# Kernel tuning notes

Measured on AMD Instinct MI355X. Metric: run time of the kernel, lower is better.

Reference implementation:

```python
import jax, jax.numpy as jnp
import numpy as np

NORMALIZE_EPS = 1e-5
INV_DELTA = 15.0
DIST_NORM_PREV = 0.5  # init value of _dist_norm_prev buffer (eval-mode constant)
SKIP_OFFSET = 2


def _l2_normalize(v, axis, eps=NORMALIZE_EPS):
    # matches torch F.normalize: v / max(||v||, eps)
    n = jnp.sqrt(jnp.sum(v * v, axis=axis, keepdims=True))
    return v / jnp.maximum(n, eps)


def setup_inputs() -> dict:
    key = jax.random.key(0)
    k1, k2 = jax.random.split(key)
    x = jax.random.normal(k1, (128, 197, 768), dtype=jnp.float32)
    emb = jnp.clip(jax.random.normal(k2, (4096, 768), dtype=jnp.float32), 0.0, None)
    emb = _l2_normalize(emb, axis=1)
    return {"x": x, "embedding": emb}


def reference(x, embedding):
    # drop CLS token -> [N, L, C] with L = H*W
    x = x[:, 1:, :]
    N, L, C = x.shape
    height = width = int(np.sqrt(L))
    # assign_words: L2-normalize tokens, cosine distance to codebook
    xn = _l2_normalize(x, axis=2)
    dist = -jnp.einsum("nlc,kc->nlk", xn, embedding)  # [N, L, K]
    inv_delta = INV_DELTA / DIST_NORM_PREV
    codes = jax.nn.softmax(-inv_delta * dist, axis=2)  # [N, L, K]
    # compute_bow: drop border tokens, mean-pool, L1-normalize
    grid = jnp.arange(height * width).reshape(height, width)
    keep = grid[SKIP_OFFSET:-SKIP_OFFSET, SKIP_OFFSET:-SKIP_OFFSET].reshape(-1)
    bow = jnp.mean(codes[:, keep, :], axis=1)  # [N, K]
    bow = bow / jnp.maximum(jnp.sum(jnp.abs(bow), axis=1, keepdims=True), NORMALIZE_EPS)
    return bow, codes
```

## Files before the change

kernel.cpp:

```cpp
#include <hip/hip_runtime.h>


typedef unsigned short ushort_t;
typedef short short8 __attribute__((ext_vector_type(8)));
typedef float float4_ __attribute__((ext_vector_type(4)));

#define M_ROWS 25088
#define N_COLS 4096
#define K_DIM  768
#define BM 128
#define BN 128
#define BK 32

__device__ __forceinline__ unsigned short f2bf_rne(float f) {
  unsigned u = __float_as_uint(f);
  unsigned r = u + 0x7fffu + ((u >> 16) & 1u);
  return (unsigned short)(r >> 16);
}
__device__ __forceinline__ float bf2f(unsigned short h) {
  return __uint_as_float(((unsigned)h) << 16);
}

__device__ __forceinline__ void gload16(const void* g, void* l) {
  __builtin_amdgcn_global_load_lds(
      (__attribute__((address_space(1))) void*)g,
      (__attribute__((address_space(3))) void*)l, 16, 0, 0);
}

__global__ void split_emb_kernel(const float* __restrict__ emb,
                                 ushort_t* __restrict__ Bh,
                                 ushort_t* __restrict__ Bl) {
  int t = blockIdx.x * 256 + threadIdx.x;
  float f = emb[t];
  unsigned short h = f2bf_rne(f);
  Bh[t] = h;
  Bl[t] = f2bf_rne(f - bf2f(h));
}

__global__ void norm_split_x_kernel(const float* __restrict__ x,
                                    ushort_t* __restrict__ Ah,
                                    ushort_t* __restrict__ Al) {
  int m = blockIdx.x;
  int n = m / 196;
  int l = m - n * 196;
  size_t src = ((size_t)n * 197 + 1 + l) * 768;
  int t = threadIdx.x;

  float v0 = x[src + t];
  float v1 = x[src + t + 256];
  float v2 = x[src + t + 512];
  float s = v0 * v0 + v1 * v1 + v2 * v2;
  #pragma unroll
  for (int off = 32; off; off >>= 1) s += __shfl_xor(s, off, 64);
  __shared__ float ws4[4];
  if ((t & 63) == 0) ws4[t >> 6] = s;
  __syncthreads();
  s = ws4[0] + ws4[1] + ws4[2] + ws4[3];
  float scale = 1.0f / fmaxf(sqrtf(s), 1e-5f);

  size_t dst = (size_t)m * 768;
  float f[3] = {v0 * scale, v1 * scale, v2 * scale};
  int idx[3] = {t, t + 256, t + 512};
  #pragma unroll
  for (int i = 0; i < 3; i++) {
    unsigned short h = f2bf_rne(f[i]);
    Ah[dst + idx[i]] = h;
    Al[dst + idx[i]] = f2bf_rne(f[i] - bf2f(h));
  }
}

__global__ __launch_bounds__(256, 4)
void gemm_exp_kernel(const ushort_t* __restrict__ Ah, const ushort_t* __restrict__ Al,
                     const ushort_t* __restrict__ Bh, const ushort_t* __restrict__ Bl,
                     float* __restrict__ codes, float* __restrict__ rowsum) {
  __shared__ __attribute__((aligned(16))) ushort_t sAh[BM * BK];
  __shared__ __attribute__((aligned(16))) ushort_t sAl[BM * BK];
  __shared__ __attribute__((aligned(16))) ushort_t sBh[BM * BK];
  __shared__ __attribute__((aligned(16))) ushort_t sBl[BM * BK];
  __shared__ float rs[BM];

  const int t = threadIdx.x;
  const int w = t >> 6;
  const int lane = t & 63;
  const int row0 = blockIdx.x * BM;
  const int col0 = blockIdx.y * BN;

  if (t < BM) rs[t] = 0.f;

  float4_ acc[4][4];
  #pragma unroll
  for (int i = 0; i < 4; i++)
    #pragma unroll
    for (int j = 0; j < 4; j++) acc[i][j] = (float4_){0.f, 0.f, 0.f, 0.f};

  const int r0 = t >> 2;
  const int c0 = (((t & 3) ^ ((r0 >> 1) & 3))) * 8;
  const ushort_t* gA = Ah + (size_t)(row0 + r0) * K_DIM + c0;
  const ushort_t* gAl_ = Al + (size_t)(row0 + r0) * K_DIM + c0;
  const ushort_t* gB = Bh + (size_t)(col0 + r0) * K_DIM + c0;
  const ushort_t* gBl_ = Bl + (size_t)(col0 + r0) * K_DIM + c0;
  const int half = 64 * K_DIM;
  const int ldsw = w * 512;

  const int rl = (w >> 1) * 64;
  const int cl = (w & 1) * 64;
  const int lq = lane >> 4;
  const int li = lane & 15;
  const int fsw = (li >> 1) & 3;
  const int abase = (rl + li) * BK + (lq ^ fsw) * 8;
  const int bbase = (cl + li) * BK + (lq ^ fsw) * 8;

  for (int kk = 0; kk < K_DIM; kk += BK) {
    __syncthreads();
    gload16(gA + kk,           sAh + ldsw);
    gload16(gA + kk + half,    sAh + 2048 + ldsw);
    gload16(gAl_ + kk,         sAl + ldsw);
    gload16(gAl_ + kk + half,  sAl + 2048 + ldsw);
    gload16(gB + kk,           sBh + ldsw);
    gload16(gB + kk + half,    sBh + 2048 + ldsw);
    gload16(gBl_ + kk,         sBl + ldsw);
    gload16(gBl_ + kk + half,  sBl + 2048 + ldsw);
    __syncthreads();

    short8 ah[4], al[4], bh[4], bl[4];
    #pragma unroll
    for (int i = 0; i < 4; i++) {
      ah[i] = *(const short8*)(sAh + abase + i * 16 * BK);
      al[i] = *(const short8*)(sAl + abase + i * 16 * BK);
      bh[i] = *(const short8*)(sBh + bbase + i * 16 * BK);
      bl[i] = *(const short8*)(sBl + bbase + i * 16 * BK);
    }
    #pragma unroll
    for (int i = 0; i < 4; i++)
      #pragma unroll
      for (int j = 0; j < 4; j++) {
        acc[i][j] = __builtin_amdgcn_mfma_f32_16x16x32_bf16(ah[i], bh[j], acc[i][j], 0, 0, 0);
        acc[i][j] = __builtin_amdgcn_mfma_f32_16x16x32_bf16(ah[i], bl[j], acc[i][j], 0, 0, 0);
        acc[i][j] = __builtin_amdgcn_mfma_f32_16x16x32_bf16(al[i], bh[j], acc[i][j], 0, 0, 0);
      }
  }

  float rsum[4][4];
  #pragma unroll
  for (int i = 0; i < 4; i++)
    #pragma unroll
    for (int r = 0; r < 4; r++) rsum[i][r] = 0.f;

  #pragma unroll
  for (int i = 0; i < 4; i++)
    #pragma unroll
    for (int j = 0; j < 4; j++)
      #pragma unroll
      for (int r = 0; r < 4; r++) {
        float e = __expf(30.0f * acc[i][j][r]);
        size_t row = (size_t)(row0 + rl + i * 16 + lq * 4 + r);
        size_t col = (size_t)(col0 + cl + j * 16 + li);
        codes[row * N_COLS + col] = e;
        rsum[i][r] += e;
      }

  #pragma unroll
  for (int i = 0; i < 4; i++)
    #pragma unroll
    for (int r = 0; r < 4; r++) {
      float v = rsum[i][r];
      v += __shfl_xor(v, 1, 64);
      v += __shfl_xor(v, 2, 64);
      v += __shfl_xor(v, 4, 64);
      v += __shfl_xor(v, 8, 64);
      if (li == 0) atomicAdd(&rs[rl + i * 16 + lq * 4 + r], v);
    }
  __syncthreads();
  if (t < BM) atomicAdd(&rowsum[row0 + t], rs[t]);
}

__global__ __launch_bounds__(256)
void rescale_bow_kernel(float* __restrict__ codes,
                        const float* __restrict__ rowsum,
                        float* __restrict__ bow_un) {
  const int bid = blockIdx.x;
  const int n = bid >> 4;
  const int g = (bid >> 2) & 3;
  const int chunk = bid & 3;
  const int t = threadIdx.x;
  const int k4 = chunk * 256 + t;
  const int l0 = g * 49;

  __shared__ float inv[49];
  __shared__ float keep[49];
  if (t < 49) {
    int l = l0 + t;
    inv[t] = 1.0f / rowsum[n * 196 + l];
    int rr = l / 14;
    int cc = l - rr * 14;
    keep[t] = (rr >= 2 && rr <= 11 && cc >= 2 && cc <= 11) ? 0.01f : 0.0f;
  }
  __syncthreads();

  float4_* base = (float4_*)(codes + (size_t)n * 196 * N_COLS)
                  + (size_t)l0 * 1024 + k4;
  float4_ acc = {0.f, 0.f, 0.f, 0.f};
  #pragma unroll
  for (int c = 0; c < 7; c++) {
    float4_ v[7];
    #pragma unroll
    for (int u = 0; u < 7; u++) v[u] = base[(size_t)(c * 7 + u) * 1024];
    #pragma unroll
    for (int u = 0; u < 7; u++) {
      int l = c * 7 + u;
      float iv = inv[l];
      v[u].x *= iv; v[u].y *= iv; v[u].z *= iv; v[u].w *= iv;
      base[(size_t)l * 1024] = v[u];
      float kf = keep[l];
      acc.x += kf * v[u].x; acc.y += kf * v[u].y;
      acc.z += kf * v[u].z; acc.w += kf * v[u].w;
    }
  }

  float* dst = bow_un + (size_t)n * N_COLS + (size_t)k4 * 4;
  atomicAdd(dst + 0, acc.x);
  atomicAdd(dst + 1, acc.y);
  atomicAdd(dst + 2, acc.z);
  atomicAdd(dst + 3, acc.w);
}

__global__ __launch_bounds__(256)
void bow_norm_kernel(const float* __restrict__ bow_un,
                     float* __restrict__ bow_out) {
  const int n = blockIdx.x;
  const int t = threadIdx.x;
  const float4_* src = (const float4_*)(bow_un + (size_t)n * N_COLS);
  float4_ v[4];
  float s = 0.f;
  #pragma unroll
  for (int i = 0; i < 4; i++) {
    v[i] = src[t + i * 256];
    s += fabsf(v[i].x) + fabsf(v[i].y) + fabsf(v[i].z) + fabsf(v[i].w);
  }
  #pragma unroll
  for (int off = 32; off; off >>= 1) s += __shfl_xor(s, off, 64);
  __shared__ float ws4[4];
  if ((t & 63) == 0) ws4[t >> 6] = s;
  __syncthreads();
  float invn = 1.0f / fmaxf(ws4[0] + ws4[1] + ws4[2] + ws4[3], 1e-5f);
  float4_* dst = (float4_*)(bow_out + (size_t)n * N_COLS);
  #pragma unroll
  for (int i = 0; i < 4; i++) {
    float4_ o = v[i];
    o.x *= invn; o.y *= invn; o.z *= invn; o.w *= invn;
    dst[t + i * 256] = o;
  }
}

extern "C" void kernel_launch(void* const* d_in, const int* in_sizes, int n_in,
                              void* d_out, int out_size, void* d_ws, size_t ws_size,
                              hipStream_t stream) {
  const float* x = (const float*)d_in[0];
  const float* emb = (const float*)d_in[1];
  float* bow_out = (float*)d_out;
  float* codes = (float*)d_out + 524288;

  char* ws = (char*)d_ws;
  ushort_t* Ah = (ushort_t*)(ws + 0);
  ushort_t* Al = (ushort_t*)(ws + 38535168);
  ushort_t* Bh = (ushort_t*)(ws + 77070336);
  ushort_t* Bl = (ushort_t*)(ws + 83361792);
  float* rowsum = (float*)(ws + 89653248);
  float* bow_un = (float*)(ws + 89753600);

  hipMemsetAsync(rowsum, 0, 25088 * 4, stream);
  hipMemsetAsync(bow_un, 0, 524288 * 4, stream);

  split_emb_kernel<<<12288, 256, 0, stream>>>(emb, Bh, Bl);
  norm_split_x_kernel<<<25088, 256, 0, stream>>>(x, Ah, Al);

  dim3 ggrid(M_ROWS / BM, N_COLS / BN);
  gemm_exp_kernel<<<ggrid, 256, 0, stream>>>(Ah, Al, Bh, Bl, codes, rowsum);

  rescale_bow_kernel<<<2048, 256, 0, stream>>>(codes, rowsum, bow_un);
  bow_norm_kernel<<<128, 256, 0, stream>>>(bow_un, bow_out);
}
```

Baseline: 1.121 ms.

## Double-buffer LDS tiles to overlap global loads with MFMA compute

The GEMM's shared-memory tiles are split into two buffers. The next K-slice is loaded with async global-to-LDS loads while the current slice is multiplied, using vmcnt waits and raw barriers in place of the two __syncthreads per step. This is meant to hide global load latency behind the split-bf16 MFMA work. LDS use doubles to 64KB and the launch bound drops to 2 blocks per CU, so occupancy falls.

```diff
diff --git a/kernel.cpp b/kernel.cpp
--- a/kernel.cpp
+++ b/kernel.cpp
@@ -11,6 +11,7 @@
 #define BM 128
 #define BN 128
 #define BK 32
+#define K_STEPS (K_DIM / BK)
 
 __device__ __forceinline__ unsigned short f2bf_rne(float f) {
   unsigned u = __float_as_uint(f);
@@ -69,14 +70,14 @@
   }
 }
 
-__global__ __launch_bounds__(256, 4)
+__global__ __launch_bounds__(256, 2)
 void gemm_exp_kernel(const ushort_t* __restrict__ Ah, const ushort_t* __restrict__ Al,
                      const ushort_t* __restrict__ Bh, const ushort_t* __restrict__ Bl,
                      float* __restrict__ codes, float* __restrict__ rowsum) {
-  __shared__ __attribute__((aligned(16))) ushort_t sAh[BM * BK];
-  __shared__ __attribute__((aligned(16))) ushort_t sAl[BM * BK];
-  __shared__ __attribute__((aligned(16))) ushort_t sBh[BM * BK];
-  __shared__ __attribute__((aligned(16))) ushort_t sBl[BM * BK];
+  __shared__ __attribute__((aligned(16))) ushort_t sAh[2][BM * BK];
+  __shared__ __attribute__((aligned(16))) ushort_t sAl[2][BM * BK];
+  __shared__ __attribute__((aligned(16))) ushort_t sBh[2][BM * BK];
+  __shared__ __attribute__((aligned(16))) ushort_t sBl[2][BM * BK];
   __shared__ float rs[BM];
 
   const int t = threadIdx.x;
@@ -110,25 +111,25 @@
   const int abase = (rl + li) * BK + (lq ^ fsw) * 8;
   const int bbase = (cl + li) * BK + (lq ^ fsw) * 8;
 
-  for (int kk = 0; kk < K_DIM; kk += BK) {
-    __syncthreads();
-    gload16(gA + kk,           sAh + ldsw);
-    gload16(gA + kk + half,    sAh + 2048 + ldsw);
-    gload16(gAl_ + kk,         sAl + ldsw);
-    gload16(gAl_ + kk + half,  sAl + 2048 + ldsw);
-    gload16(gB + kk,           sBh + ldsw);
-    gload16(gB + kk + half,    sBh + 2048 + ldsw);
-    gload16(gBl_ + kk,         sBl + ldsw);
-    gload16(gBl_ + kk + half,  sBl + 2048 + ldsw);
-    __syncthreads();
-
+  auto issue = [&](int b, int kk) {
+    gload16(gA + kk,           &sAh[b][ldsw]);
+    gload16(gA + kk + half,    &sAh[b][2048 + ldsw]);
+    gload16(gAl_ + kk,         &sAl[b][ldsw]);
+    gload16(gAl_ + kk + half,  &sAl[b][2048 + ldsw]);
+    gload16(gB + kk,           &sBh[b][ldsw]);
+    gload16(gB + kk + half,    &sBh[b][2048 + ldsw]);
+    gload16(gBl_ + kk,         &sBl[b][ldsw]);
+    gload16(gBl_ + kk + half,  &sBl[b][2048 + ldsw]);
+  };
+
+  auto compute = [&](int b) {
     short8 ah[4], al[4], bh[4], bl[4];
     #pragma unroll
     for (int i = 0; i < 4; i++) {
-      ah[i] = *(const short8*)(sAh + abase + i * 16 * BK);
-      al[i] = *(const short8*)(sAl + abase + i * 16 * BK);
-      bh[i] = *(const short8*)(sBh + bbase + i * 16 * BK);
-      bl[i] = *(const short8*)(sBl + bbase + i * 16 * BK);
+      ah[i] = *(const short8*)(&sAh[b][abase + i * 16 * BK]);
+      al[i] = *(const short8*)(&sAl[b][abase + i * 16 * BK]);
+      bh[i] = *(const short8*)(&sBh[b][bbase + i * 16 * BK]);
+      bl[i] = *(const short8*)(&sBl[b][bbase + i * 16 * BK]);
     }
     #pragma unroll
     for (int i = 0; i < 4; i++)
@@ -138,7 +139,41 @@
         acc[i][j] = __builtin_amdgcn_mfma_f32_16x16x32_bf16(ah[i], bl[j], acc[i][j], 0, 0, 0);
         acc[i][j] = __builtin_amdgcn_mfma_f32_16x16x32_bf16(al[i], bh[j], acc[i][j], 0, 0, 0);
       }
-  }
+  };
+
+  issue(0, 0);
+
+  #pragma unroll 1
+  for (int ks = 0; ks < K_STEPS - 2; ks += 2) {
+    issue(1, (ks + 1) * BK);
+    asm volatile("s_waitcnt vmcnt(8)" ::: "memory");
+    __builtin_amdgcn_s_barrier();
+    asm volatile("" ::: "memory");
+    compute(0);
+    asm volatile("" ::: "memory");
+    __builtin_amdgcn_s_barrier();
+
+    issue(0, (ks + 2) * BK);
+    asm volatile("s_waitcnt vmcnt(8)" ::: "memory");
+    __builtin_amdgcn_s_barrier();
+    asm volatile("" ::: "memory");
+    compute(1);
+    asm volatile("" ::: "memory");
+    __builtin_amdgcn_s_barrier();
+  }
+
+  issue(1, (K_STEPS - 1) * BK);
+  asm volatile("s_waitcnt vmcnt(8)" ::: "memory");
+  __builtin_amdgcn_s_barrier();
+  asm volatile("" ::: "memory");
+  compute(0);
+  asm volatile("" ::: "memory");
+  __builtin_amdgcn_s_barrier();
+
+  asm volatile("s_waitcnt vmcnt(0)" ::: "memory");
+  __builtin_amdgcn_s_barrier();
+  asm volatile("" ::: "memory");
+  compute(1);
 
   float rsum[4][4];
   #pragma unroll
```

Result: faster. 1.057 ms (-5.7%).
